# Performance work log

Hardware: AMD Instinct MI355X
Metric: run time of the kernel (lower is better)

Reference implementation:

```python
import jax, jax.numpy as jnp
import numpy as np

T, D, H, L = 4096, 1024, 512, 2  # seq_len, input_size, per-direction hidden (state_size//2), num_layers


def setup_inputs() -> dict:
    key = jax.random.key(0)
    inp = {"emb": jax.random.normal(key, (T, D), jnp.float32) * 0.1}
    k = 1
    for d in ("fwd", "bwd"):
        for l in range(L):
            in_sz = D if l == 0 else H
            inp[f"{d}_Wih_{l}"] = jax.random.normal(jax.random.fold_in(key, k), (4 * H, in_sz), jnp.float32) * float(1.0 / np.sqrt(in_sz)); k += 1
            inp[f"{d}_Whh_{l}"] = jax.random.normal(jax.random.fold_in(key, k), (4 * H, H), jnp.float32) * float(1.0 / np.sqrt(H)); k += 1
            inp[f"{d}_bih_{l}"] = jnp.zeros((4 * H,), jnp.float32)
            inp[f"{d}_bhh_{l}"] = jnp.zeros((4 * H,), jnp.float32)
    return inp


def _lstm_stack(xs, params):
    """Run a stack of unidirectional LSTM layers over xs [T, in].
    Returns (final cells [L,H], final hiddens [L,H], top-layer outputs [T,H])."""
    cTs, hTs = [], []
    for Wih, Whh, bih, bhh in params:
        h0 = jnp.zeros((Wih.shape[0] // 4,), xs.dtype)

        def step(carry, x, Wih=Wih, Whh=Whh, b=bih + bhh):
            h, c = carry
            g = Wih @ x + Whh @ h + b          # [4H], torch LSTMCell gate order i,f,g,o
            i, f, gg, o = jnp.split(g, 4)
            c = jax.nn.sigmoid(f) * c + jax.nn.sigmoid(i) * jnp.tanh(gg)
            h = jax.nn.sigmoid(o) * jnp.tanh(c)
            return (h, c), h

        (hT, cT), xs = jax.lax.scan(step, (h0, h0), xs)
        cTs.append(cT)
        hTs.append(hT)
    return jnp.stack(cTs), jnp.stack(hTs), xs


def reference(emb,
              fwd_Wih_0, fwd_Whh_0, fwd_bih_0, fwd_bhh_0,
              fwd_Wih_1, fwd_Whh_1, fwd_bih_1, fwd_bhh_1,
              bwd_Wih_0, bwd_Whh_0, bwd_bih_0, bwd_bhh_0,
              bwd_Wih_1, bwd_Whh_1, bwd_bih_1, bwd_bhh_1):
    fparams = [(fwd_Wih_0, fwd_Whh_0, fwd_bih_0, fwd_bhh_0),
               (fwd_Wih_1, fwd_Whh_1, fwd_bih_1, fwd_bhh_1)]
    bparams = [(bwd_Wih_0, bwd_Whh_0, bwd_bih_0, bwd_bhh_0),
               (bwd_Wih_1, bwd_Whh_1, bwd_bih_1, bwd_bhh_1)]
    fc, fh, fy = _lstm_stack(emb, fparams)          # forward pass over sequence
    bc, bh, by = _lstm_stack(emb[::-1], bparams)    # backward pass over reversed sequence
    cell_memories = jnp.concatenate([fc, bc], axis=-1)   # [L, state_size]
    hidden_states = jnp.concatenate([fh, bh], axis=-1)   # [L, state_size]
    outputs = jnp.concatenate([fy, by[::-1]], axis=-1)   # [T, state_size] per-token final-layer states
    return (cell_memories, hidden_states, outputs)
```

## Files before the change

### kernel.cpp

```cpp
#include <hip/hip_runtime.h>
#include <cstdint>
#include <cstddef>

#define T_SEQ 4096
#define HSZ   512
#define NGATE 2048
#define DIN   1024
#define NB0   32
#define HB0   16
#define NB1   64
#define HB1   8
#define S_SLOT 16
#define CH0   68

typedef unsigned long long u64;
typedef unsigned int u32;

__device__ __forceinline__ u64 exld(const u64* p) {
  return __hip_atomic_load(p, __ATOMIC_RELAXED, __HIP_MEMORY_SCOPE_AGENT);
}
__device__ __forceinline__ void exst(u64* p, u64 v) {
  __hip_atomic_store(p, v, __ATOMIC_RELAXED, __HIP_MEMORY_SCOPE_AGENT);
}
__device__ __forceinline__ int pgld(const u32* p) {
  return (int)__hip_atomic_load(p, __ATOMIC_RELAXED, __HIP_MEMORY_SCOPE_AGENT);
}
__device__ __forceinline__ void pgst(u32* p, u32 v) {
  __hip_atomic_store(p, v, __ATOMIC_RELAXED, __HIP_MEMORY_SCOPE_AGENT);
}

__device__ __forceinline__ float frcp(float x) { return __builtin_amdgcn_rcpf(x); }
__device__ __forceinline__ float fsig(float x) { return frcp(1.f + __expf(-x)); }
__device__ __forceinline__ float ftnh(float x) { return 1.f - 2.f * frcp(1.f + __expf(2.f * x)); }

__global__ void init_sync_kernel(u64* ex, u32* prog) {
  const int tid = blockIdx.x * blockDim.x + threadIdx.x;
  if (tid < 2 * 2 * S_SLOT * HSZ) exst(&ex[tid], 0ull);
  if (tid < 2 * (NB0 + NB1)) pgst(&prog[tid], 0u);
}

__global__ __launch_bounds__(256, 2)
void gemm_bias_kernel(const float* __restrict__ Xf, const float* __restrict__ Xb,
                      const float* __restrict__ Wf, const float* __restrict__ Wb,
                      const float* __restrict__ bif, const float* __restrict__ bhf,
                      const float* __restrict__ bib, const float* __restrict__ bhb,
                      float* __restrict__ Pf, float* __restrict__ Pb, int K)
{
  const int dir = blockIdx.z;
  const float* X  = dir ? Xb  : Xf;
  const float* W  = dir ? Wb  : Wf;
  const float* bi = dir ? bib : bif;
  const float* bh = dir ? bhb : bhf;
  float* P        = dir ? Pb  : Pf;

  const int m0 = blockIdx.x * 128;
  const int n0 = blockIdx.y * 128;
  const int tid = threadIdx.x;
  const int lr = tid >> 1;
  const int lk = (tid & 1) * 8;

  __shared__ float As[16*128];
  __shared__ float Bs[16*128];

  float acc[8][8];
  #pragma unroll
  for (int i = 0; i < 8; ++i)
    #pragma unroll
    for (int j = 0; j < 8; ++j) acc[i][j] = 0.f;

  for (int k0 = 0; k0 < K; k0 += 16) {
    const float4 a0 = *(const float4*)(X + (size_t)(m0+lr)*K + k0 + lk);
    const float4 a1 = *(const float4*)(X + (size_t)(m0+lr)*K + k0 + lk + 4);
    const float4 b0 = *(const float4*)(W + (size_t)(n0+lr)*K + k0 + lk);
    const float4 b1 = *(const float4*)(W + (size_t)(n0+lr)*K + k0 + lk + 4);
    __syncthreads();
    As[(lk+0)*128+lr]=a0.x; As[(lk+1)*128+lr]=a0.y; As[(lk+2)*128+lr]=a0.z; As[(lk+3)*128+lr]=a0.w;
    As[(lk+4)*128+lr]=a1.x; As[(lk+5)*128+lr]=a1.y; As[(lk+6)*128+lr]=a1.z; As[(lk+7)*128+lr]=a1.w;
    Bs[(lk+0)*128+lr]=b0.x; Bs[(lk+1)*128+lr]=b0.y; Bs[(lk+2)*128+lr]=b0.z; Bs[(lk+3)*128+lr]=b0.w;
    Bs[(lk+4)*128+lr]=b1.x; Bs[(lk+5)*128+lr]=b1.y; Bs[(lk+6)*128+lr]=b1.z; Bs[(lk+7)*128+lr]=b1.w;
    __syncthreads();
    #pragma unroll
    for (int kk = 0; kk < 16; ++kk) {
      const float4 A0 = *(const float4*)(As + kk*128 + (tid&15)*8);
      const float4 A1 = *(const float4*)(As + kk*128 + (tid&15)*8 + 4);
      const float4 B0 = *(const float4*)(Bs + kk*128 + (tid>>4)*8);
      const float4 B1 = *(const float4*)(Bs + kk*128 + (tid>>4)*8 + 4);
      const float av[8] = {A0.x,A0.y,A0.z,A0.w,A1.x,A1.y,A1.z,A1.w};
      const float bv[8] = {B0.x,B0.y,B0.z,B0.w,B1.x,B1.y,B1.z,B1.w};
      #pragma unroll
      for (int i = 0; i < 8; ++i)
        #pragma unroll
        for (int j = 0; j < 8; ++j) acc[i][j] += av[i]*bv[j];
    }
  }
  const int tm = m0 + (tid&15)*8;
  const int tn = n0 + (tid>>4)*8;
  #pragma unroll
  for (int i = 0; i < 8; ++i) {
    #pragma unroll
    for (int j = 0; j < 8; ++j) {
      const int n = tn + j;
      P[(size_t)(tm+i)*NGATE + n] = acc[i][j] + bi[n] + bh[n];
    }
  }
}

__global__ __launch_bounds__(512, 2)
void fused_recur_kernel(const float* __restrict__ Whh0_f, const float* __restrict__ Whh0_b,
                        const float* __restrict__ Wih1_f, const float* __restrict__ Whh1_f,
                        const float* __restrict__ bih1_f, const float* __restrict__ bhh1_f,
                        const float* __restrict__ Wih1_b, const float* __restrict__ Whh1_b,
                        const float* __restrict__ bih1_b, const float* __restrict__ bhh1_b,
                        const float* __restrict__ P_f, const float* __restrict__ P_b,
                        u64* ex0, u64* ex1, u32* prog0, u32* prog1,
                        float* __restrict__ out)
{
  const int bx  = blockIdx.x;
  const int tid = threadIdx.x;
  const int lane = tid & 63;
  const int wv   = tid >> 6;

  __shared__ float xh[2][16*CH0];

  if (bx < 2*NB0) {
    const int dir = (bx >= NB0) ? 1 : 0;
    const int b   = bx - dir*NB0;
    const float* Whh = dir ? Whh0_b : Whh0_f;
    const float* P   = dir ? P_b    : P_f;
    u64* exS   = ex0 + (size_t)dir*S_SLOT*HSZ;
    u32* prS   = prog0 + dir*NB0;
    u32* prL1  = prog1 + dir*NB1;

    const int g  = lane & 3;
    const int el = (lane >> 2) & 1;
    const int cc = lane >> 3;
    const int e  = wv*2 + el;
    const int grow = g*HSZ + b*HB0 + e;
    const bool red0 = (cc == 0);
    const bool pub  = red0 && (g == 0);

    float4 w[16];
    {
      const float4* wp = (const float4*)(Whh + (size_t)grow*HSZ + cc*64);
      #pragma unroll
      for (int j = 0; j < 16; ++j) w[j] = wp[j];
    }

    float creg = 0.f;
    float pv = 0.f;
    if (red0) pv = P[(size_t)(dir ? (T_SEQ-1) : 0)*NGATE + grow];

    for (int t = 0; t < T_SEQ; ++t) {
      if ((t & 7) == 0) {
        if (tid >= 64 && tid < 64+NB0)        { while (pgld(&prS[tid-64])  < t-4) {} }
        else if (tid >= 96 && tid < 96+NB1)   { while (pgld(&prL1[tid-96]) < t-4) {} }
      }
      {
        const u64* sp = exS + (size_t)(t & (S_SLOT-1))*HSZ + tid;
        u64 v;
        do { v = exld(sp); } while ((u32)(v >> 32) != (u32)t);
        xh[t & 1][(tid>>6)*CH0 + (tid & 63)] = __uint_as_float((u32)v);
      }
      __syncthreads();
      if (tid == 0) pgst(&prS[b], (u32)(t+1));
      float pvn = 0.f;
      if (red0 && t+1 < T_SEQ) pvn = P[(size_t)(dir ? (T_SEQ-2-t) : (t+1))*NGATE + grow];
      const float4* h4 = (const float4*)(xh[t & 1] + cc*CH0);
      float a0=0.f, a1=0.f, a2=0.f, a3=0.f;
      #pragma unroll
      for (int j = 0; j < 16; j += 4) {
        const float4 h0 = h4[j], h1 = h4[j+1], h2 = h4[j+2], h3 = h4[j+3];
        a0 += w[j].x*h0.x   + w[j].y*h0.y   + w[j].z*h0.z   + w[j].w*h0.w;
        a1 += w[j+1].x*h1.x + w[j+1].y*h1.y + w[j+1].z*h1.z + w[j+1].w*h1.w;
        a2 += w[j+2].x*h2.x + w[j+2].y*h2.y + w[j+2].z*h2.z + w[j+2].w*h2.w;
        a3 += w[j+3].x*h3.x + w[j+3].y*h3.y + w[j+3].z*h3.z + w[j+3].w*h3.w;
      }
      float acc = (a0+a1)+(a2+a3);
      acc += __shfl_xor(acc, 8);
      acc += __shfl_xor(acc, 16);
      acc += __shfl_xor(acc, 32);
      const float val = acc + pv;
      pv = pvn;
      const float av = (g == 2) ? ftnh(val) : fsig(val);
      const float f1 = __shfl_xor(av, 1);
      const float f2 = __shfl_xor(av, 2);
      const float f3 = __shfl_xor(av, 3);
      if (pub) {
        creg = f1*creg + av*f2;
        const float hnew = f3*ftnh(creg);
        const int hidx = b*HB0 + e;
        const u64 pkt = ((u64)(u32)(t+1) << 32) | (u64)__float_as_uint(hnew);
        exst(exS + (size_t)((t+1) & (S_SLOT-1))*HSZ + hidx, pkt);
        if (t == T_SEQ-1) {
          out[dir*HSZ + hidx]        = creg;
          out[2048 + dir*HSZ + hidx] = hnew;
        }
      }
    }
  } else {
    const int r   = bx - 2*NB0;
    const int dir = (r >= NB1) ? 1 : 0;
    const int b   = r - dir*NB1;
    const float* Wih = dir ? Wih1_b : Wih1_f;
    const float* Whh = dir ? Whh1_b : Whh1_f;
    const float* bi  = dir ? bih1_b : bih1_f;
    const float* bh  = dir ? bhh1_b : bhh1_f;
    u64* exX = ex0 + (size_t)dir*S_SLOT*HSZ;
    u64* exS = ex1 + (size_t)dir*S_SLOT*HSZ;
    u32* prS = prog1 + dir*NB1;

    const int g  = lane & 3;
    const int cc = lane >> 2;
    const int e  = wv;
    const int grow = g*HSZ + b*HB1 + e;
    const bool red0 = (cc == 0);
    const bool pub  = red0 && (g == 0);

    float4 w[16];
    {
      const float* wsrc = (cc < 8) ? (Wih + (size_t)grow*HSZ + cc*64)
                                   : (Whh + (size_t)grow*HSZ + (cc-8)*64);
      const float4* wp = (const float4*)wsrc;
      #pragma unroll
      for (int j = 0; j < 16; ++j) w[j] = wp[j];
    }
    float brow = 0.f;
    if (red0) brow = bi[grow] + bh[grow];

    float creg = 0.f;
    u64 xpf = exld(exX + (size_t)(1 & (S_SLOT-1))*HSZ + tid);

    for (int t = 0; t < T_SEQ; ++t) {
      if ((t & 7) == 0 && tid >= 64 && tid < 64+NB1) { while (pgld(&prS[tid-64]) < t-4) {} }
      {
        const u64* px = exX + (size_t)((t+1) & (S_SLOT-1))*HSZ + tid;
        const u64* ph = exS + (size_t)(t & (S_SLOT-1))*HSZ + tid;
        u64 vx = xpf; bool okx = ((u32)(vx >> 32) == (u32)(t+1));
        float hv = 0.f; bool okh = false;
        do {
          if (!okx) { u64 v = exld(px); if ((u32)(v >> 32) == (u32)(t+1)) { vx = v; okx = true; } }
          if (!okh) { u64 v = exld(ph); if ((u32)(v >> 32) == (u32)t)     { hv = __uint_as_float((u32)v); okh = true; } }
        } while (!(okx && okh));
        xh[t & 1][(tid>>6)*CH0 + (tid & 63)]       = __uint_as_float((u32)vx);
        xh[t & 1][(8 + (tid>>6))*CH0 + (tid & 63)] = hv;
      }
      __syncthreads();
      if (tid == 0) pgst(&prS[b], (u32)(t+1));
      xpf = exld(exX + (size_t)((t+2) & (S_SLOT-1))*HSZ + tid);
      const float4* v4 = (const float4*)(xh[t & 1] + cc*CH0);
      float a0=0.f, a1=0.f, a2=0.f, a3=0.f;
      #pragma unroll
      for (int j = 0; j < 16; j += 4) {
        const float4 h0 = v4[j], h1 = v4[j+1], h2 = v4[j+2], h3 = v4[j+3];
        a0 += w[j].x*h0.x   + w[j].y*h0.y   + w[j].z*h0.z   + w[j].w*h0.w;
        a1 += w[j+1].x*h1.x + w[j+1].y*h1.y + w[j+1].z*h1.z + w[j+1].w*h1.w;
        a2 += w[j+2].x*h2.x + w[j+2].y*h2.y + w[j+2].z*h2.z + w[j+2].w*h2.w;
        a3 += w[j+3].x*h3.x + w[j+3].y*h3.y + w[j+3].z*h3.z + w[j+3].w*h3.w;
      }
      float acc = (a0+a1)+(a2+a3);
      acc += __shfl_xor(acc, 4);
      acc += __shfl_xor(acc, 8);
      acc += __shfl_xor(acc, 16);
      acc += __shfl_xor(acc, 32);
      const float val = acc + brow;
      const float av = (g == 2) ? ftnh(val) : fsig(val);
      const float f1 = __shfl_xor(av, 1);
      const float f2 = __shfl_xor(av, 2);
      const float f3 = __shfl_xor(av, 3);
      if (pub) {
        creg = f1*creg + av*f2;
        const float hnew = f3*ftnh(creg);
        const int hidx = b*HB1 + e;
        const u64 pkt = ((u64)(u32)(t+1) << 32) | (u64)__float_as_uint(hnew);
        exst(exS + (size_t)((t+1) & (S_SLOT-1))*HSZ + hidx, pkt);
        const int trow = dir ? (T_SEQ-1-t) : t;
        out[4096 + (size_t)trow*1024 + dir*HSZ + hidx] = hnew;
        if (t == T_SEQ-1) {
          out[1024 + dir*HSZ + hidx]        = creg;
          out[2048 + 1024 + dir*HSZ + hidx] = hnew;
        }
      }
    }
  }
}

extern "C" void kernel_launch(void* const* d_in, const int* in_sizes, int n_in,
                              void* d_out, int out_size, void* d_ws, size_t ws_size,
                              hipStream_t stream)
{
  const float* emb   = (const float*)d_in[0];
  const float* fWih0 = (const float*)d_in[1];
  const float* fWhh0 = (const float*)d_in[2];
  const float* fbih0 = (const float*)d_in[3];
  const float* fbhh0 = (const float*)d_in[4];
  const float* fWih1 = (const float*)d_in[5];
  const float* fWhh1 = (const float*)d_in[6];
  const float* fbih1 = (const float*)d_in[7];
  const float* fbhh1 = (const float*)d_in[8];
  const float* bWih0 = (const float*)d_in[9];
  const float* bWhh0 = (const float*)d_in[10];
  const float* bbih0 = (const float*)d_in[11];
  const float* bbhh0 = (const float*)d_in[12];
  const float* bWih1 = (const float*)d_in[13];
  const float* bWhh1 = (const float*)d_in[14];
  const float* bbih1 = (const float*)d_in[15];
  const float* bbhh1 = (const float*)d_in[16];
  float* out = (float*)d_out;

  float* P_f = (float*)d_ws;
  float* P_b = P_f + (size_t)T_SEQ*NGATE;
  u64*   ex0 = (u64*)(P_b + (size_t)T_SEQ*NGATE);
  u64*   ex1 = ex0 + 2*S_SLOT*HSZ;
  u32*   prog0 = (u32*)(ex1 + 2*S_SLOT*HSZ);
  u32*   prog1 = prog0 + 2*NB0;

  init_sync_kernel<<<32, 1024, 0, stream>>>(ex0, prog0);

  gemm_bias_kernel<<<dim3(32,16,2), 256, 0, stream>>>(
      emb, emb, fWih0, bWih0, fbih0, fbhh0, bbih0, bbhh0, P_f, P_b, DIN);

  fused_recur_kernel<<<2*NB0 + 2*NB1, 512, 0, stream>>>(
      fWhh0, bWhh0,
      fWih1, fWhh1, fbih1, fbhh1,
      bWih1, bWhh1, bbih1, bbhh1,
      P_f, P_b, ex0, ex1, prog0, prog1, out);
}
```

Baseline: 7.091 ms.

## Poll exchange slots with 32-byte vector loads and reload weights from cache each step

The h/x exchange buffers are now polled by 128 threads, each using two dwordx4 cache-bypassing loads over four packets, instead of one 8-byte atomic load per thread. After 4096 failed polls it falls back to per-element atomic loads. Weights are no longer held in registers across the time loop; they are reloaded from global memory every step, and waves_per_eu is pinned to 2. The goal is to cut polling latency and instruction count, and to free registers. The cost is a per-step weight reload from L2, plus reliance on 16-byte loads not tearing against the 8-byte tag/value stores.

```diff
diff --git a/kernel.cpp b/kernel.cpp
--- a/kernel.cpp
+++ b/kernel.cpp
@@ -27,6 +27,39 @@
 }
 __device__ __forceinline__ void pgst(u32* p, u32 v) {
   __hip_atomic_store(p, v, __ATOMIC_RELAXED, __HIP_MEMORY_SCOPE_AGENT);
+}
+
+__device__ __forceinline__ void exld16x2(const u64* p, ulonglong2& A, ulonglong2& B) {
+  asm volatile("global_load_dwordx4 %0, %2, off sc0 sc1\n"
+               "global_load_dwordx4 %1, %2, off offset:16 sc0 sc1\n"
+               "s_waitcnt vmcnt(0)"
+               : "=&v"(A), "=&v"(B) : "v"(p) : "memory");
+}
+
+__device__ __forceinline__ void pollw(const u64* base, u32 tag, bool& fast, float4& out) {
+  if (fast) {
+    int it = 0;
+    for (;;) {
+      ulonglong2 A, B;
+      exld16x2(base, A, B);
+      if ((u32)(A.x >> 32) == tag && (u32)(A.y >> 32) == tag &&
+          (u32)(B.x >> 32) == tag && (u32)(B.y >> 32) == tag) {
+        out = make_float4(__uint_as_float((u32)A.x), __uint_as_float((u32)A.y),
+                          __uint_as_float((u32)B.x), __uint_as_float((u32)B.y));
+        return;
+      }
+      if (++it > 4096) { fast = false; break; }
+    }
+  }
+  u64 v0=0, v1=0, v2=0, v3=0; bool o0=false, o1=false, o2=false, o3=false;
+  do {
+    if (!o0) { u64 v = exld(base+0); if ((u32)(v>>32) == tag) { v0 = v; o0 = true; } }
+    if (!o1) { u64 v = exld(base+1); if ((u32)(v>>32) == tag) { v1 = v; o1 = true; } }
+    if (!o2) { u64 v = exld(base+2); if ((u32)(v>>32) == tag) { v2 = v; o2 = true; } }
+    if (!o3) { u64 v = exld(base+3); if ((u32)(v>>32) == tag) { v3 = v; o3 = true; } }
+  } while (!(o0 && o1 && o2 && o3));
+  out = make_float4(__uint_as_float((u32)v0), __uint_as_float((u32)v1),
+                    __uint_as_float((u32)v2), __uint_as_float((u32)v3));
 }
 
 __device__ __forceinline__ float frcp(float x) { return __builtin_amdgcn_rcpf(x); }
@@ -105,7 +138,7 @@
   }
 }
 
-__global__ __launch_bounds__(512, 2)
+__global__ __launch_bounds__(512, 2) __attribute__((amdgpu_waves_per_eu(2, 2)))
 void fused_recur_kernel(const float* __restrict__ Whh0_f, const float* __restrict__ Whh0_b,
                         const float* __restrict__ Wih1_f, const float* __restrict__ Whh1_f,
                         const float* __restrict__ bih1_f, const float* __restrict__ bhh1_f,
@@ -120,7 +153,7 @@
   const int lane = tid & 63;
   const int wv   = tid >> 6;
 
-  __shared__ float xh[2][16*CH0];
+  __shared__ __align__(16) float xh[2][16*CH0];
 
   if (bx < 2*NB0) {
     const int dir = (bx >= NB0) ? 1 : 0;
@@ -138,31 +171,29 @@
     const int grow = g*HSZ + b*HB0 + e;
     const bool red0 = (cc == 0);
     const bool pub  = red0 && (g == 0);
-
-    float4 w[16];
-    {
-      const float4* wp = (const float4*)(Whh + (size_t)grow*HSZ + cc*64);
-      #pragma unroll
-      for (int j = 0; j < 16; ++j) w[j] = wp[j];
-    }
+    const float4* wp = (const float4*)(Whh + (size_t)grow*HSZ + cc*64);
 
     float creg = 0.f;
     float pv = 0.f;
     if (red0) pv = P[(size_t)(dir ? (T_SEQ-1) : 0)*NGATE + grow];
+    bool fastH = true;
 
     for (int t = 0; t < T_SEQ; ++t) {
       if ((t & 7) == 0) {
-        if (tid >= 64 && tid < 64+NB0)        { while (pgld(&prS[tid-64])  < t-4) {} }
-        else if (tid >= 96 && tid < 96+NB1)   { while (pgld(&prL1[tid-96]) < t-4) {} }
-      }
-      {
-        const u64* sp = exS + (size_t)(t & (S_SLOT-1))*HSZ + tid;
-        u64 v;
-        do { v = exld(sp); } while ((u32)(v >> 32) != (u32)t);
-        xh[t & 1][(tid>>6)*CH0 + (tid & 63)] = __uint_as_float((u32)v);
+        if (tid >= 256 && tid < 256+NB0)      { while (pgld(&prS[tid-256])  < t-4) {} }
+        else if (tid >= 320 && tid < 320+NB1) { while (pgld(&prL1[tid-320]) < t-4) {} }
+      }
+      float4 wr[16];
+      #pragma unroll
+      for (int j = 0; j < 16; ++j) wr[j] = wp[j];
+      if (tid < 128) {
+        const int s = 4*tid;
+        float4 hv;
+        pollw(exS + (size_t)(t & (S_SLOT-1))*HSZ + s, (u32)t, fastH, hv);
+        *(float4*)&xh[t & 1][(s>>6)*CH0 + (s&63)] = hv;
       }
       __syncthreads();
-      if (tid == 0) pgst(&prS[b], (u32)(t+1));
+      if (tid == 256) pgst(&prS[b], (u32)(t+1));
       float pvn = 0.f;
       if (red0 && t+1 < T_SEQ) pvn = P[(size_t)(dir ? (T_SEQ-2-t) : (t+1))*NGATE + grow];
       const float4* h4 = (const float4*)(xh[t & 1] + cc*CH0);
@@ -170,10 +201,10 @@
       #pragma unroll
       for (int j = 0; j < 16; j += 4) {
         const float4 h0 = h4[j], h1 = h4[j+1], h2 = h4[j+2], h3 = h4[j+3];
-        a0 += w[j].x*h0.x   + w[j].y*h0.y   + w[j].z*h0.z   + w[j].w*h0.w;
-        a1 += w[j+1].x*h1.x + w[j+1].y*h1.y + w[j+1].z*h1.z + w[j+1].w*h1.w;
-        a2 += w[j+2].x*h2.x + w[j+2].y*h2.y + w[j+2].z*h2.z + w[j+2].w*h2.w;
-        a3 += w[j+3].x*h3.x + w[j+3].y*h3.y + w[j+3].z*h3.z + w[j+3].w*h3.w;
+        a0 += wr[j].x*h0.x   + wr[j].y*h0.y   + wr[j].z*h0.z   + wr[j].w*h0.w;
+        a1 += wr[j+1].x*h1.x + wr[j+1].y*h1.y + wr[j+1].z*h1.z + wr[j+1].w*h1.w;
+        a2 += wr[j+2].x*h2.x + wr[j+2].y*h2.y + wr[j+2].z*h2.z + wr[j+2].w*h2.w;
+        a3 += wr[j+3].x*h3.x + wr[j+3].y*h3.y + wr[j+3].z*h3.z + wr[j+3].w*h3.w;
       }
       float acc = (a0+a1)+(a2+a3);
       acc += __shfl_xor(acc, 8);
@@ -215,47 +246,42 @@
     const int grow = g*HSZ + b*HB1 + e;
     const bool red0 = (cc == 0);
     const bool pub  = red0 && (g == 0);
-
-    float4 w[16];
-    {
-      const float* wsrc = (cc < 8) ? (Wih + (size_t)grow*HSZ + cc*64)
-                                   : (Whh + (size_t)grow*HSZ + (cc-8)*64);
-      const float4* wp = (const float4*)wsrc;
-      #pragma unroll
-      for (int j = 0; j < 16; ++j) w[j] = wp[j];
-    }
+    const float4* wp = (const float4*)((cc < 8) ? (Wih + (size_t)grow*HSZ + cc*64)
+                                                : (Whh + (size_t)grow*HSZ + (cc-8)*64));
+
     float brow = 0.f;
     if (red0) brow = bi[grow] + bh[grow];
 
     float creg = 0.f;
-    u64 xpf = exld(exX + (size_t)(1 & (S_SLOT-1))*HSZ + tid);
+    bool fastX = true, fastH = true;
 
     for (int t = 0; t < T_SEQ; ++t) {
-      if ((t & 7) == 0 && tid >= 64 && tid < 64+NB1) { while (pgld(&prS[tid-64]) < t-4) {} }
-      {
-        const u64* px = exX + (size_t)((t+1) & (S_SLOT-1))*HSZ + tid;
-        const u64* ph = exS + (size_t)(t & (S_SLOT-1))*HSZ + tid;
-        u64 vx = xpf; bool okx = ((u32)(vx >> 32) == (u32)(t+1));
-        float hv = 0.f; bool okh = false;
-        do {
-          if (!okx) { u64 v = exld(px); if ((u32)(v >> 32) == (u32)(t+1)) { vx = v; okx = true; } }
-          if (!okh) { u64 v = exld(ph); if ((u32)(v >> 32) == (u32)t)     { hv = __uint_as_float((u32)v); okh = true; } }
-        } while (!(okx && okh));
-        xh[t & 1][(tid>>6)*CH0 + (tid & 63)]       = __uint_as_float((u32)vx);
-        xh[t & 1][(8 + (tid>>6))*CH0 + (tid & 63)] = hv;
+      if ((t & 7) == 0 && tid >= 256 && tid < 256+NB1) { while (pgld(&prS[tid-256]) < t-4) {} }
+      float4 wr[16];
+      #pragma unroll
+      for (int j = 0; j < 16; ++j) wr[j] = wp[j];
+      if (tid < 128) {
+        const int s = 4*tid;
+        float4 xv;
+        pollw(exX + (size_t)((t+1) & (S_SLOT-1))*HSZ + s, (u32)(t+1), fastX, xv);
+        *(float4*)&xh[t & 1][(s>>6)*CH0 + (s&63)] = xv;
+      } else if (tid < 256) {
+        const int s = 4*(tid-128);
+        float4 hv;
+        pollw(exS + (size_t)(t & (S_SLOT-1))*HSZ + s, (u32)t, fastH, hv);
+        *(float4*)&xh[t & 1][(8 + (s>>6))*CH0 + (s&63)] = hv;
       }
       __syncthreads();
-      if (tid == 0) pgst(&prS[b], (u32)(t+1));
-      xpf = exld(exX + (size_t)((t+2) & (S_SLOT-1))*HSZ + tid);
+      if (tid == 256) pgst(&prS[b], (u32)(t+1));
       const float4* v4 = (const float4*)(xh[t & 1] + cc*CH0);
       float a0=0.f, a1=0.f, a2=0.f, a3=0.f;
       #pragma unroll
       for (int j = 0; j < 16; j += 4) {
         const float4 h0 = v4[j], h1 = v4[j+1], h2 = v4[j+2], h3 = v4[j+3];
-        a0 += w[j].x*h0.x   + w[j].y*h0.y   + w[j].z*h0.z   + w[j].w*h0.w;
-        a1 += w[j+1].x*h1.x + w[j+1].y*h1.y + w[j+1].z*h1.z + w[j+1].w*h1.w;
-        a2 += w[j+2].x*h2.x + w[j+2].y*h2.y + w[j+2].z*h2.z + w[j+2].w*h2.w;
-        a3 += w[j+3].x*h3.x + w[j+3].y*h3.y + w[j+3].z*h3.z + w[j+3].w*h3.w;
+        a0 += wr[j].x*h0.x   + wr[j].y*h0.y   + wr[j].z*h0.z   + wr[j].w*h0.w;
+        a1 += wr[j+1].x*h1.x + wr[j+1].y*h1.y + wr[j+1].z*h1.z + wr[j+1].w*h1.w;
+        a2 += wr[j+2].x*h2.x + wr[j+2].y*h2.y + wr[j+2].z*h2.z + wr[j+2].w*h2.w;
+        a3 += wr[j+3].x*h3.x + wr[j+3].y*h3.y + wr[j+3].z*h3.z + wr[j+3].w*h3.w;
       }
       float acc = (a0+a1)+(a2+a3);
       acc += __shfl_xor(acc, 4);
```

Result: slower. 15.16 ms (+113.8%).
